# Kernel optimization log

Hardware: AMD Instinct MI355X
Metric: run time of the kernel (lower is better)

The kernel has to match this reference:

```python
import jax, jax.numpy as jnp
import numpy as np
import math

B = 64
N = 2048
EMBED_DIM = 128
N_HEADS = 8
VAL_DIM = EMBED_DIM // N_HEADS  # 16
KEY_DIM = VAL_DIM               # key_dim defaults to val_dim
CLIP = True
NORM = 1.0 / math.sqrt(KEY_DIM)


def _uniform_param(k, shape):
    # torch init: uniform(-stdv, stdv) with stdv = 1/sqrt(size(-1))
    stdv = 1.0 / math.sqrt(shape[-1])
    return jax.random.uniform(k, shape, jnp.float32, -stdv, stdv)


def setup_inputs() -> dict:
    key = jax.random.key(0)
    ks = jax.random.split(key, 11)
    h = jax.random.normal(ks[0], (B, N, EMBED_DIM), jnp.float32)
    adj_c = jax.random.randint(ks[1], (B, N, N), 0, 2).astype(jnp.float32)
    phone_set = jax.random.randint(ks[2], (B,), 1, N - 1)
    return dict(
        h=h, adj_c=adj_c, phone_set=phone_set,
        Wq_bf=_uniform_param(ks[3], (EMBED_DIM, KEY_DIM)),
        Wk_bf=_uniform_param(ks[4], (EMBED_DIM, KEY_DIM)),
        Wv_bf=_uniform_param(ks[5], (EMBED_DIM, VAL_DIM)),
        Wo_bf=_uniform_param(ks[6], (VAL_DIM, EMBED_DIM)),
        Wq_af=_uniform_param(ks[7], (EMBED_DIM, KEY_DIM)),
        Wk_af=_uniform_param(ks[8], (EMBED_DIM, KEY_DIM)),
        Wv_af=_uniform_param(ks[9], (EMBED_DIM, VAL_DIM)),
        Wo_af=_uniform_param(ks[10], (VAL_DIM, EMBED_DIM)),
    )


def _attend(h, h_phone, adj_row, pos_mask, Wq, Wk, Wv, Wo):
    # h: (B,N,D), h_phone: (B,D), adj_row: (B,N), pos_mask: (B,N) bool
    Q = h_phone @ Wq                              # (B,K)
    K = jnp.einsum('bnd,dk->bnk', h, Wk)          # (B,N,K)
    V = jnp.einsum('bnd,dk->bnk', h, Wv)          # (B,N,V)
    compat = NORM * jnp.einsum('bk,bnk->bn', Q, K)
    if CLIP:
        compat = 10.0 * jnp.tanh(compat)
    valid = pos_mask & (adj_row != 0)
    # masked stable softmax over valid positions; fully-masked rows -> zeros
    mx = jnp.max(jnp.where(valid, compat, -jnp.inf), axis=-1, keepdims=True)
    mx = jnp.where(jnp.isfinite(mx), mx, 0.0)
    e = jnp.where(valid, jnp.exp(compat - mx), 0.0)
    s = jnp.sum(e, axis=-1, keepdims=True)
    attn = (e / jnp.where(s > 0, s, 1.0)) * adj_row   # matches attn * adj slice
    head = jnp.einsum('bn,bnk->bk', attn, V)          # (B,V)
    return head @ Wo                                  # (B,D)


def reference(h, adj_c, phone_set, Wq_bf, Wk_bf, Wv_bf, Wo_bf,
              Wq_af, Wk_af, Wv_af, Wo_af):
    b, n, d = h.shape
    bidx = jnp.arange(b)
    h_phone = h[bidx, phone_set]        # (B,D) single query per graph
    adj_row = adj_c[bidx, phone_set]    # (B,N) adjacency row of phone node
    pos = jnp.arange(n)[None, :]
    mask_bf = pos < phone_set[:, None]   # indices [0, phone)
    mask_af = pos >= phone_set[:, None]  # indices [phone, N)
    g_bf = _attend(h, h_phone, adj_row, mask_bf, Wq_bf, Wk_bf, Wv_bf, Wo_bf)
    g_af = _attend(h, h_phone, adj_row, mask_af, Wq_af, Wk_af, Wv_af, Wo_af)
    return (g_bf, g_af)
```

## Files before the change

### kernel.cpp

```cpp
#include <hip/hip_runtime.h>
#include <math.h>

#define BB 64
#define NN 2048
#define DD 128
#define KD 16
#define NORMF 0.25f
#define CHUNK 32
#define PSTRIDE 260
#define LOG2E 1.4426950408889634f

__device__ __forceinline__ void wave_lds_fence() {
    asm volatile("s_waitcnt lgkmcnt(0)" ::: "memory");
    __builtin_amdgcn_wave_barrier();
}

template <int P>
__global__ __launch_bounds__(256, 2)
void attn_main(const float* __restrict__ h,
               const float* __restrict__ adj,
               const int*   __restrict__ phone,
               const float* __restrict__ Wq_bf, const float* __restrict__ Wk_bf,
               const float* __restrict__ Wq_af, const float* __restrict__ Wk_af,
               float* __restrict__ ws)
{
    constexpr int K = 16 / P;
    const int tid  = threadIdx.x;
    const int wid  = tid >> 6;
    const int lane = tid & 63;
    const int half = lane >> 5;
    const int l    = lane & 31;
    const int dbase = 4 * l;

    const int xcd  = blockIdx.x & 7;
    const int slot = blockIdx.x >> 3;
    const int b    = xcd + 8 * (slot / P);
    const int bip  = slot % P;
    const int ph   = phone[b];

    __shared__ float hp[DD];
    __shared__ float qpart[32][8];
    __shared__ float q[2][KD];
    __shared__ float w_s[2][DD];
    __shared__ float part[4][CHUNK][33];
    __shared__ float ea_s[4][CHUNK];
    __shared__ float red_h[4][2][DD];
    __shared__ float red_s[4][2];

    const float* hb     = h + (size_t)b * NN * DD;
    const float* adjrow = adj + ((size_t)b * NN + ph) * NN;
    const int chbase    = (bip * 4 + wid) * K;

    float adjv[K];
    #pragma unroll
    for (int c = 0; c < K; ++c) adjv[c] = adjrow[(chbase + c) * CHUNK + l];

    if (tid < DD) hp[tid] = hb[(size_t)ph * DD + tid];

    const int pair = tid >> 3, sub = tid & 7;
    const int brq = pair >> 4, kq = pair & 15;
    const float* Wq = brq ? Wq_af : Wq_bf;
    float wqr[16];
    #pragma unroll
    for (int i = 0; i < 16; ++i) wqr[i] = Wq[(sub * 16 + i) * KD + kq];

    const int brw = tid >> 7, dw = tid & 127;
    const float* Wk = brw ? Wk_af : Wk_bf;
    float wkr[KD];
    #pragma unroll
    for (int k = 0; k < KD; ++k) wkr[k] = Wk[dw * KD + k];

    auto load_chunk = [&](float4* hv, unsigned long long mask, int n0) {
        #pragma unroll
        for (int t = 0; t < 16; ++t) {
            const int r = 2 * t + half;
            hv[t] = make_float4(0.f, 0.f, 0.f, 0.f);
            if ((mask >> r) & 1ull)
                hv[t] = *(const float4*)(hb + (size_t)(n0 + r) * DD + dbase);
        }
    };

    float4 hv0[16], hv1[16];
    {
        const unsigned long long m0 = __ballot(adjv[0] != 0.f);
        load_chunk(hv0, m0, (chbase + 0) * CHUNK);
        if (K > 1) {
            const unsigned long long m1 = __ballot(adjv[1] != 0.f);
            load_chunk(hv1, m1, (chbase + 1) * CHUNK);
        }
    }

    __syncthreads();
    {
        float acc = 0.f;
        #pragma unroll
        for (int i = 0; i < 16; ++i) acc += hp[sub * 16 + i] * wqr[i];
        qpart[pair][sub] = acc;
    }
    __syncthreads();
    if (tid < 32) {
        float acc = 0.f;
        #pragma unroll
        for (int i = 0; i < 8; ++i) acc += qpart[tid][i];
        q[tid >> 4][tid & 15] = acc;
    }
    __syncthreads();
    {
        float acc = 0.f;
        #pragma unroll
        for (int k = 0; k < KD; ++k) acc += wkr[k] * q[brw][k];
        w_s[brw][dw] = NORMF * acc;
    }
    __syncthreads();

    const float4 wbf = *(const float4*)(&w_s[0][dbase]);
    const float4 waf = *(const float4*)(&w_s[1][dbase]);

    float sbf = 0.f, saf = 0.f;
    float hgbf[4] = {0, 0, 0, 0}, hgaf[4] = {0, 0, 0, 0};

    auto softexp = [](float p) {
        const float t = __builtin_amdgcn_exp2f(2.f * LOG2E * p);
        return __builtin_amdgcn_exp2f(-20.f * LOG2E * __builtin_amdgcn_rcpf(t + 1.f));
    };

    auto compute_chunk = [&](int n0, const float4* hv, float adjc) {
        #pragma unroll
        for (int t = 0; t < 16; ++t) {
            const int r = 2 * t + half;
            const float4 w = ((n0 + r) >= ph) ? waf : wbf;
            part[wid][r][l] = hv[t].x * w.x + hv[t].y * w.y + hv[t].z * w.z + hv[t].w * w.w;
        }
        wave_lds_fence();

        float a0 = 0.f, a1 = 0.f, a2 = 0.f, a3 = 0.f;
        #pragma unroll
        for (int j = 0; j < 32; j += 4) {
            a0 += part[wid][l][j];
            a1 += part[wid][l][j + 1];
            a2 += part[wid][l][j + 2];
            a3 += part[wid][l][j + 3];
        }
        const float p = (a0 + a1) + (a2 + a3);
        const float e = softexp(p);
        const float es = (adjc != 0.f) ? e : 0.f;
        const float ea = es * adjc;
        const bool rowaf = (n0 + l) >= ph;
        sbf += rowaf ? 0.f : es;
        saf += rowaf ? es : 0.f;
        if (lane < 32) ea_s[wid][l] = ea;
        wave_lds_fence();

        #pragma unroll
        for (int t = 0; t < 16; ++t) {
            const int r = 2 * t + half;
            const float ear = ea_s[wid][r];
            const bool af = (n0 + r) >= ph;
            const float eb = af ? 0.f : ear;
            const float ef = af ? ear : 0.f;
            hgbf[0] += eb * hv[t].x; hgbf[1] += eb * hv[t].y;
            hgbf[2] += eb * hv[t].z; hgbf[3] += eb * hv[t].w;
            hgaf[0] += ef * hv[t].x; hgaf[1] += ef * hv[t].y;
            hgaf[2] += ef * hv[t].z; hgaf[3] += ef * hv[t].w;
        }
    };

    compute_chunk((chbase + 0) * CHUNK, hv0, adjv[0]);
    if (K > 1) compute_chunk((chbase + 1) * CHUNK, hv1, adjv[1]);

    #pragma unroll
    for (int cc = 2; cc < K; cc += 2) {
        const unsigned long long m0 = __ballot(adjv[cc] != 0.f);
        load_chunk(hv0, m0, (chbase + cc) * CHUNK);
        if (cc + 1 < K) {
            const unsigned long long m1 = __ballot(adjv[cc + 1] != 0.f);
            load_chunk(hv1, m1, (chbase + cc + 1) * CHUNK);
        }
        compute_chunk((chbase + cc) * CHUNK, hv0, adjv[cc]);
        if (cc + 1 < K) compute_chunk((chbase + cc + 1) * CHUNK, hv1, adjv[cc + 1]);
    }

    #pragma unroll
    for (int m = 1; m <= 16; m <<= 1) {
        sbf += __shfl_xor(sbf, m, 64);
        saf += __shfl_xor(saf, m, 64);
    }
    #pragma unroll
    for (int i = 0; i < 4; ++i) {
        hgbf[i] += __shfl_xor(hgbf[i], 32, 64);
        hgaf[i] += __shfl_xor(hgaf[i], 32, 64);
    }
    if (lane < 32) {
        #pragma unroll
        for (int i = 0; i < 4; ++i) {
            red_h[wid][0][dbase + i] = hgbf[i];
            red_h[wid][1][dbase + i] = hgaf[i];
        }
    }
    if (lane == 0) { red_s[wid][0] = sbf; red_s[wid][1] = saf; }
    __syncthreads();

    {
        const int br = tid >> 7, d = tid & 127;
        float* op = ws + (size_t)(b * P + bip) * PSTRIDE;
        op[br * DD + d] = red_h[0][br][d] + red_h[1][br][d] + red_h[2][br][d] + red_h[3][br][d];
        if (tid < 2)
            op[2 * DD + tid] = red_s[0][tid] + red_s[1][tid] + red_s[2][tid] + red_s[3][tid];
    }
}

template <int P>
__global__ __launch_bounds__(256)
void finalize_kernel(const float* __restrict__ Wv_bf, const float* __restrict__ Wo_bf,
                     const float* __restrict__ Wv_af, const float* __restrict__ Wo_af,
                     const float* __restrict__ ws, float* __restrict__ out)
{
    const int b = blockIdx.x;
    const int tid = threadIdx.x;
    __shared__ float hs[2][DD];
    __shared__ float ssum[2];
    __shared__ float hpart[32][8];
    __shared__ float head[2][KD];

    const int pair = tid >> 3, sub = tid & 7;
    const int brv = pair >> 4, kv = pair & 15;
    const float* Wv = brv ? Wv_af : Wv_bf;
    float wvr[16];
    #pragma unroll
    for (int i = 0; i < 16; ++i) wvr[i] = Wv[(sub * 16 + i) * KD + kv];

    const int br2 = tid >> 7, j = tid & 127;
    const float* Wo = br2 ? Wo_af : Wo_bf;
    float wor[KD];
    #pragma unroll
    for (int k = 0; k < KD; ++k) wor[k] = Wo[k * DD + j];

    const float* base = ws + (size_t)b * P * PSTRIDE;
    {
        float acc = 0.f;
        #pragma unroll
        for (int p = 0; p < P; ++p) acc += base[(size_t)p * PSTRIDE + br2 * DD + j];
        hs[br2][j] = acc;
    }
    if (tid < 2) {
        float acc = 0.f;
        #pragma unroll
        for (int p = 0; p < P; ++p) acc += base[(size_t)p * PSTRIDE + 2 * DD + tid];
        ssum[tid] = acc;
    }
    __syncthreads();

    {
        float acc = 0.f;
        #pragma unroll
        for (int i = 0; i < 16; ++i) acc += hs[brv][sub * 16 + i] * wvr[i];
        hpart[pair][sub] = acc;
    }
    __syncthreads();
    if (tid < 32) {
        float acc = 0.f;
        #pragma unroll
        for (int i = 0; i < 8; ++i) acc += hpart[tid][i];
        head[tid >> 4][tid & 15] = acc;
    }
    __syncthreads();

    {
        const float s = ssum[br2];
        const float inv = (s > 0.f) ? 1.f / s : 0.f;
        float acc = 0.f;
        #pragma unroll
        for (int k = 0; k < KD; ++k) acc += head[br2][k] * wor[k];
        out[br2 * BB * DD + b * DD + j] = acc * inv;
    }
}

extern "C" void kernel_launch(void* const* d_in, const int* in_sizes, int n_in,
                              void* d_out, int out_size, void* d_ws, size_t ws_size,
                              hipStream_t stream) {
    const float* h     = (const float*)d_in[0];
    const float* adj   = (const float*)d_in[1];
    const int*   phone = (const int*)d_in[2];
    const float* Wq_bf = (const float*)d_in[3];
    const float* Wk_bf = (const float*)d_in[4];
    const float* Wv_bf = (const float*)d_in[5];
    const float* Wo_bf = (const float*)d_in[6];
    const float* Wq_af = (const float*)d_in[7];
    const float* Wk_af = (const float*)d_in[8];
    const float* Wv_af = (const float*)d_in[9];
    const float* Wo_af = (const float*)d_in[10];

    float* out = (float*)d_out;
    float* ws  = (float*)d_ws;

    int P = 8;
    while (P > 1 && (size_t)BB * P * PSTRIDE * sizeof(float) > ws_size) P >>= 1;

    switch (P) {
    case 8:
        attn_main<8><<<BB * 8, 256, 0, stream>>>(h, adj, phone, Wq_bf, Wk_bf, Wq_af, Wk_af, ws);
        finalize_kernel<8><<<BB, 256, 0, stream>>>(Wv_bf, Wo_bf, Wv_af, Wo_af, ws, out);
        break;
    case 4:
        attn_main<4><<<BB * 4, 256, 0, stream>>>(h, adj, phone, Wq_bf, Wk_bf, Wq_af, Wk_af, ws);
        finalize_kernel<4><<<BB, 256, 0, stream>>>(Wv_bf, Wo_bf, Wv_af, Wo_af, ws, out);
        break;
    case 2:
        attn_main<2><<<BB * 2, 256, 0, stream>>>(h, adj, phone, Wq_bf, Wk_bf, Wq_af, Wk_af, ws);
        finalize_kernel<2><<<BB, 256, 0, stream>>>(Wv_bf, Wo_bf, Wv_af, Wo_af, ws, out);
        break;
    default:
        attn_main<1><<<BB, 256, 0, stream>>>(h, adj, phone, Wq_bf, Wk_bf, Wq_af, Wk_af, ws);
        finalize_kernel<1><<<BB, 256, 0, stream>>>(Wv_bf, Wo_bf, Wv_af, Wo_af, ws, out);
        break;
    }
}
```

Baseline: 17.28 us.

## Move Wv projection into main kernel with 512-thread blocks and smaller partials

Blocks grow from 4 to 8 waves, and the batch split drops from 8 to 4 blocks per graph, keeping 2 chunks per wave. Each block now reduces its per-wave weighted-h sums in LDS and applies Wv itself, writing only 34 floats per partial instead of 260. This shrinks workspace traffic and leaves the finalize kernel with just the Wo projection. Wq/Wk are no longer prefetched into registers before the h loads, so those global reads now sit on the critical path after the sync, and the extra Wv work runs in the main kernel's tail.

```diff
diff --git a/kernel.cpp b/kernel.cpp
--- a/kernel.cpp
+++ b/kernel.cpp
@@ -7,7 +7,7 @@
 #define KD 16
 #define NORMF 0.25f
 #define CHUNK 32
-#define PSTRIDE 260
+#define PSTRIDE 36
 #define LOG2E 1.4426950408889634f
 
 __device__ __forceinline__ void wave_lds_fence() {
@@ -16,15 +16,16 @@
 }
 
 template <int P>
-__global__ __launch_bounds__(256, 2)
+__global__ __launch_bounds__(512, 2)
 void attn_main(const float* __restrict__ h,
                const float* __restrict__ adj,
                const int*   __restrict__ phone,
                const float* __restrict__ Wq_bf, const float* __restrict__ Wk_bf,
+               const float* __restrict__ Wv_bf, const float* __restrict__ Wv_af,
                const float* __restrict__ Wq_af, const float* __restrict__ Wk_af,
                float* __restrict__ ws)
 {
-    constexpr int K = 16 / P;
+    constexpr int K = 64 / (8 * P);
     const int tid  = threadIdx.x;
     const int wid  = tid >> 6;
     const int lane = tid & 63;
@@ -39,36 +40,25 @@
     const int ph   = phone[b];
 
     __shared__ float hp[DD];
-    __shared__ float qpart[32][8];
+    __shared__ float qpart[32][16];
     __shared__ float q[2][KD];
     __shared__ float w_s[2][DD];
-    __shared__ float part[4][CHUNK][33];
-    __shared__ float ea_s[4][CHUNK];
-    __shared__ float red_h[4][2][DD];
-    __shared__ float red_s[4][2];
+    __shared__ float part[8][CHUNK][33];
+    __shared__ float ea_s[8][CHUNK];
+    __shared__ float red_h[8][2][DD];
+    __shared__ float red_s[8][2];
+    __shared__ float vpart[32][16];
+    __shared__ float s2[2];
 
     const float* hb     = h + (size_t)b * NN * DD;
     const float* adjrow = adj + ((size_t)b * NN + ph) * NN;
-    const int chbase    = (bip * 4 + wid) * K;
+    const int chbase    = (bip * 8 + wid) * K;
 
     float adjv[K];
     #pragma unroll
     for (int c = 0; c < K; ++c) adjv[c] = adjrow[(chbase + c) * CHUNK + l];
 
     if (tid < DD) hp[tid] = hb[(size_t)ph * DD + tid];
-
-    const int pair = tid >> 3, sub = tid & 7;
-    const int brq = pair >> 4, kq = pair & 15;
-    const float* Wq = brq ? Wq_af : Wq_bf;
-    float wqr[16];
-    #pragma unroll
-    for (int i = 0; i < 16; ++i) wqr[i] = Wq[(sub * 16 + i) * KD + kq];
-
-    const int brw = tid >> 7, dw = tid & 127;
-    const float* Wk = brw ? Wk_af : Wk_bf;
-    float wkr[KD];
-    #pragma unroll
-    for (int k = 0; k < KD; ++k) wkr[k] = Wk[dw * KD + k];
 
     auto load_chunk = [&](float4* hv, unsigned long long mask, int n0) {
         #pragma unroll
@@ -90,25 +80,34 @@
         }
     }
 
+    const int pair = tid >> 4, sub = tid & 15;
+    const int brq = pair >> 4, kq = pair & 15;
+
     __syncthreads();
     {
-        float acc = 0.f;
-        #pragma unroll
-        for (int i = 0; i < 16; ++i) acc += hp[sub * 16 + i] * wqr[i];
+        const float* Wq = brq ? Wq_af : Wq_bf;
+        float acc = 0.f;
+        #pragma unroll
+        for (int i = 0; i < 8; ++i) {
+            const int d = sub * 8 + i;
+            acc += hp[d] * Wq[d * KD + kq];
+        }
         qpart[pair][sub] = acc;
     }
     __syncthreads();
     if (tid < 32) {
         float acc = 0.f;
         #pragma unroll
-        for (int i = 0; i < 8; ++i) acc += qpart[tid][i];
+        for (int i = 0; i < 16; ++i) acc += qpart[tid][i];
         q[tid >> 4][tid & 15] = acc;
     }
     __syncthreads();
-    {
-        float acc = 0.f;
-        #pragma unroll
-        for (int k = 0; k < KD; ++k) acc += wkr[k] * q[brw][k];
+    if (tid < 256) {
+        const int brw = tid >> 7, dw = tid & 127;
+        const float* Wk = brw ? Wk_af : Wk_bf;
+        float acc = 0.f;
+        #pragma unroll
+        for (int k = 0; k < KD; ++k) acc += Wk[dw * KD + k] * q[brw][k];
         w_s[brw][dw] = NORMF * acc;
     }
     __syncthreads();
@@ -200,78 +199,77 @@
     if (lane == 0) { red_s[wid][0] = sbf; red_s[wid][1] = saf; }
     __syncthreads();
 
+    if (tid < 256) {
+        const int brh = tid >> 7, dh = tid & 127;
+        float acc = 0.f;
+        #pragma unroll
+        for (int w = 0; w < 8; ++w) acc += red_h[w][brh][dh];
+        w_s[brh][dh] = acc;
+    }
+    if (tid < 2) {
+        float acc = 0.f;
+        #pragma unroll
+        for (int w = 0; w < 8; ++w) acc += red_s[w][tid];
+        s2[tid] = acc;
+    }
+    __syncthreads();
+
     {
-        const int br = tid >> 7, d = tid & 127;
-        float* op = ws + (size_t)(b * P + bip) * PSTRIDE;
-        op[br * DD + d] = red_h[0][br][d] + red_h[1][br][d] + red_h[2][br][d] + red_h[3][br][d];
-        if (tid < 2)
-            op[2 * DD + tid] = red_s[0][tid] + red_s[1][tid] + red_s[2][tid] + red_s[3][tid];
-    }
+        const float* Wv = brq ? Wv_af : Wv_bf;
+        float acc = 0.f;
+        #pragma unroll
+        for (int i = 0; i < 8; ++i) {
+            const int d = sub * 8 + i;
+            acc += w_s[brq][d] * Wv[d * KD + kq];
+        }
+        vpart[pair][sub] = acc;
+    }
+    __syncthreads();
+
+    float* op = ws + (size_t)(b * P + bip) * PSTRIDE;
+    if (tid < 32) {
+        float acc = 0.f;
+        #pragma unroll
+        for (int i = 0; i < 16; ++i) acc += vpart[tid][i];
+        op[tid] = acc;
+    }
+    if (tid < 2) op[32 + tid] = s2[tid];
 }
 
 template <int P>
 __global__ __launch_bounds__(256)
-void finalize_kernel(const float* __restrict__ Wv_bf, const float* __restrict__ Wo_bf,
-                     const float* __restrict__ Wv_af, const float* __restrict__ Wo_af,
+void finalize_kernel(const float* __restrict__ Wo_bf, const float* __restrict__ Wo_af,
                      const float* __restrict__ ws, float* __restrict__ out)
 {
     const int b = blockIdx.x;
     const int tid = threadIdx.x;
-    __shared__ float hs[2][DD];
+    __shared__ float head[2][KD];
     __shared__ float ssum[2];
-    __shared__ float hpart[32][8];
-    __shared__ float head[2][KD];
-
-    const int pair = tid >> 3, sub = tid & 7;
-    const int brv = pair >> 4, kv = pair & 15;
-    const float* Wv = brv ? Wv_af : Wv_bf;
-    float wvr[16];
-    #pragma unroll
-    for (int i = 0; i < 16; ++i) wvr[i] = Wv[(sub * 16 + i) * KD + kv];
-
-    const int br2 = tid >> 7, j = tid & 127;
-    const float* Wo = br2 ? Wo_af : Wo_bf;
-    float wor[KD];
-    #pragma unroll
-    for (int k = 0; k < KD; ++k) wor[k] = Wo[k * DD + j];
 
     const float* base = ws + (size_t)b * P * PSTRIDE;
+    if (tid < 32) {
+        float acc = 0.f;
+        #pragma unroll
+        for (int p = 0; p < P; ++p) acc += base[p * PSTRIDE + tid];
+        head[tid >> 4][tid & 15] = acc;
+    }
+    if (tid < 2) {
+        float acc = 0.f;
+        #pragma unroll
+        for (int p = 0; p < P; ++p) acc += base[p * PSTRIDE + 32 + tid];
+        ssum[tid] = acc;
+    }
+    __syncthreads();
+
     {
-        float acc = 0.f;
-        #pragma unroll
-        for (int p = 0; p < P; ++p) acc += base[(size_t)p * PSTRIDE + br2 * DD + j];
-        hs[br2][j] = acc;
-    }
-    if (tid < 2) {
-        float acc = 0.f;
-        #pragma unroll
-        for (int p = 0; p < P; ++p) acc += base[(size_t)p * PSTRIDE + 2 * DD + tid];
-        ssum[tid] = acc;
-    }
-    __syncthreads();
-
-    {
-        float acc = 0.f;
-        #pragma unroll
-        for (int i = 0; i < 16; ++i) acc += hs[brv][sub * 16 + i] * wvr[i];
-        hpart[pair][sub] = acc;
-    }
-    __syncthreads();
-    if (tid < 32) {
-        float acc = 0.f;
-        #pragma unroll
-        for (int i = 0; i < 8; ++i) acc += hpart[tid][i];
-        head[tid >> 4][tid & 15] = acc;
-    }
-    __syncthreads();
-
-    {
-        const float s = ssum[br2];
+        const int br = tid >> 7, j = tid & 127;
+        const float s = ssum[br];
         const float inv = (s > 0.f) ? 1.f / s : 0.f;
-        float acc = 0.f;
-        #pragma unroll
-        for (int k = 0; k < KD; ++k) acc += head[br2][k] * wor[k];
-        out[br2 * BB * DD + b * DD + j] = acc * inv;
+        const float* Wo = br ? Wo_af : Wo_bf;
+        float acc = 0.f;
+        #pragma unroll
+        for (int k = 0; k < KD; ++k) acc += head[br][k] * Wo[k * DD + j];
+        out[br * BB * DD + b * DD + j] = acc * inv;
     }
 }
 
@@ -293,25 +291,24 @@
     float* out = (float*)d_out;
     float* ws  = (float*)d_ws;
 
-    int P = 8;
+    int P = 4;
     while (P > 1 && (size_t)BB * P * PSTRIDE * sizeof(float) > ws_size) P >>= 1;
 
     switch (P) {
-    case 8:
-        attn_main<8><<<BB * 8, 256, 0, stream>>>(h, adj, phone, Wq_bf, Wk_bf, Wq_af, Wk_af, ws);
-        finalize_kernel<8><<<BB, 256, 0, stream>>>(Wv_bf, Wo_bf, Wv_af, Wo_af, ws, out);
-        break;
     case 4:
-        attn_main<4><<<BB * 4, 256, 0, stream>>>(h, adj, phone, Wq_bf, Wk_bf, Wq_af, Wk_af, ws);
-        finalize_kernel<4><<<BB, 256, 0, stream>>>(Wv_bf, Wo_bf, Wv_af, Wo_af, ws, out);
+        attn_main<4><<<BB * 4, 512, 0, stream>>>(h, adj, phone, Wq_bf, Wk_bf, Wv_bf, Wv_af,
+                                                 Wq_af, Wk_af, ws);
+        finalize_kernel<4><<<BB, 256, 0, stream>>>(Wo_bf, Wo_af, ws, out);
         break;
     case 2:
-        attn_main<2><<<BB * 2, 256, 0, stream>>>(h, adj, phone, Wq_bf, Wk_bf, Wq_af, Wk_af, ws);
-        finalize_kernel<2><<<BB, 256, 0, stream>>>(Wv_bf, Wo_bf, Wv_af, Wo_af, ws, out);
+        attn_main<2><<<BB * 2, 512, 0, stream>>>(h, adj, phone, Wq_bf, Wk_bf, Wv_bf, Wv_af,
+                                                 Wq_af, Wk_af, ws);
+        finalize_kernel<2><<<BB, 256, 0, stream>>>(Wo_bf, Wo_af, ws, out);
         break;
     default:
-        attn_main<1><<<BB, 256, 0, stream>>>(h, adj, phone, Wq_bf, Wk_bf, Wq_af, Wk_af, ws);
-        finalize_kernel<1><<<BB, 256, 0, stream>>>(Wv_bf, Wo_bf, Wv_af, Wo_af, ws, out);
+        attn_main<1><<<BB, 512, 0, stream>>>(h, adj, phone, Wq_bf, Wk_bf, Wv_bf, Wv_af,
+                                             Wq_af, Wk_af, ws);
+        finalize_kernel<1><<<BB, 256, 0, stream>>>(Wo_bf, Wo_af, ws, out);
         break;
     }
 }
```

Measured after the change: 19.04 us. +10.2%, slower.
